# Kernel optimization log

Measured on AMD Instinct MI355X. Metric: run time of the kernel, lower is better.

## Reference

```python
import jax, jax.numpy as jnp
import numpy as np

B, T, H, O = 256, 512, 1024, 256


def setup_inputs() -> dict:
    key = jax.random.key(0)
    k0, k1, k2, k3, k4 = jax.random.split(key, 5)
    scale_ih = 1.0 / np.sqrt(1 + H)
    scale_ho = 1.0 / np.sqrt(H)
    return {
        "x": jax.random.normal(k0, (B, T), dtype=jnp.float32),
        "W_ih": jax.random.normal(k1, (1 + H, H), dtype=jnp.float32) * scale_ih,
        "b_ih": jax.random.normal(k2, (H,), dtype=jnp.float32) * scale_ih,
        "W_ho": jax.random.normal(k3, (H, O), dtype=jnp.float32) * scale_ho,
        "b_ho": jax.random.normal(k4, (O,), dtype=jnp.float32) * scale_ho,
    }


def reference(x, W_ih, b_ih, W_ho, b_ho):
    # Elman RNN cell: hidden = tanh(W_ih @ [x_t; h]); output = W_ho @ h_T.
    # Only the final timestep's output is returned by the original module,
    # so h2o is applied once to the final hidden state (identical math).
    batch = x.shape[0]
    h0 = jnp.zeros((batch, W_ih.shape[1]), dtype=x.dtype)

    def step(h, x_t):  # x_t: [B], h: [B, H]
        combined = jnp.concatenate([x_t[:, None], h], axis=1)  # [B, 1+H]
        h_new = jnp.tanh(combined @ W_ih + b_ih)               # [B, H]
        return h_new, None

    h_final, _ = jax.lax.scan(step, h0, x.T)  # scan over T
    return h_final @ W_ho + b_ho              # [B, O]
```

## Files before the change

kernel.cpp:

```cpp
#include <hip/hip_runtime.h>
#include <hip/hip_bf16.h>


#define Bsz 256
#define Tn  512
#define Hn  1024
#define On  256

typedef __attribute__((ext_vector_type(8))) _Float16 f16x8;
typedef __attribute__((ext_vector_type(4))) float f32x4;
typedef __attribute__((ext_vector_type(4))) int   i32x4;
typedef __attribute__((ext_vector_type(2))) int   i32x2;

__device__ __forceinline__ unsigned f2h(float f) {
    _Float16 h = (_Float16)f;
    union { _Float16 h; unsigned short s; } u; u.h = h;
    return (unsigned)u.s;
}

__device__ __forceinline__ f16x8 as_f16x8(i32x4 v) {
    union { i32x4 i; f16x8 h; } u; u.i = v; return u.h;
}

__device__ __forceinline__ float fast_tanh(float x) {
    float xc = fminf(fmaxf(x, -9.f), 9.f);
    float e  = __builtin_amdgcn_exp2f(xc * 2.8853900817779268f);
    return (e - 1.f) * __builtin_amdgcn_rcpf(e + 1.f);
}

#define MFMA_F16 __builtin_amdgcn_mfma_f32_16x16x32_f16

__device__ __forceinline__ void stage_quarter(const short* __restrict__ hsrc,
                                              short* __restrict__ htile,
                                              int row0, int cg, int kq,
                                              int lane, unsigned tag) {
    const int half = lane >> 5, gl = lane & 31, r0 = cg * 8;
    const short* a0 = hsrc + (size_t)(row0 + r0 + 0 + half) * Hn + kq * 256 + gl * 8;
    const short* a1 = hsrc + (size_t)(row0 + r0 + 2 + half) * Hn + kq * 256 + gl * 8;
    const short* a2 = hsrc + (size_t)(row0 + r0 + 4 + half) * Hn + kq * 256 + gl * 8;
    const short* a3 = hsrc + (size_t)(row0 + r0 + 6 + half) * Hn + kq * 256 + gl * 8;
    i32x4 t0, t1, t2, t3;
    for (;;) {
        asm volatile("global_load_dwordx4 %0, %1, off sc0 sc1"
                     : "=&v"(t0) : "v"(a0) : "memory");
        asm volatile("global_load_dwordx4 %0, %1, off sc0 sc1"
                     : "=&v"(t1) : "v"(a1) : "memory");
        asm volatile("global_load_dwordx4 %0, %1, off sc0 sc1"
                     : "=&v"(t2) : "v"(a2) : "memory");
        asm volatile("global_load_dwordx4 %0, %1, off sc0 sc1"
                     : "=&v"(t3) : "v"(a3) : "memory");
        asm volatile("s_waitcnt vmcnt(0)" ::: "memory");
        unsigned bad = 0;
#pragma unroll
        for (int e = 0; e < 4; ++e)
            bad |= (unsigned)(t0[e] ^ tag) | (unsigned)(t1[e] ^ tag) |
                   (unsigned)(t2[e] ^ tag) | (unsigned)(t3[e] ^ tag);
        if (!__any(bad & 1u)) break;
    }
    i32x4 tv[4] = {t0, t1, t2, t3};
#pragma unroll
    for (int p = 0; p < 4; ++p) {
        int row = r0 + 2 * p + half;
        int g   = kq * 32 + gl;
        int idx = row * 128 + (g ^ (row & 7));
        *(i32x4*)(htile + idx * 8) = tv[p];
    }
}

__global__ __launch_bounds__(512, 2) void rnn_kernel(
    const float* __restrict__ x,
    const float* __restrict__ W_ih,
    const float* __restrict__ b_ih,
    const float* __restrict__ W_ho,
    const float* __restrict__ b_ho,
    float* __restrict__ out,
    short* __restrict__ hbuf)
{
    const int tid  = threadIdx.x;
    const int lane = tid & 63;
    const int w    = tid >> 6;
    const int cg   = w >> 2;
    const int kq   = w & 3;
    const int q    = lane >> 4;
    const int n    = lane & 15;

    const int i = blockIdx.x & 15;
    const int j = blockIdx.x >> 4;
    const int colbase = j * 128 + cg * 64;
    const int owncol  = colbase + kq * 16 + 4 * q;
    const int row0    = i * 16;

    __shared__ float x_lds[16][Tn + 1];
    __shared__ short htile[16 * Hn];
    __shared__ float redbuf[2][8 * 3 * 256];
    __shared__ int   pairflag[4];

    if (tid < 4) pairflag[tid] = 0;

    for (int idx = tid; idx < 16 * Tn; idx += 512) {
        int r = idx >> 9, tt = idx & (Tn - 1);
        x_lds[r][tt] = x[(row0 + r) * Tn + tt];
    }

    f16x8 wfrag[32];
#pragma unroll
    for (int mt = 0; mt < 4; ++mt)
#pragma unroll
        for (int ks = 0; ks < 8; ++ks) {
#pragma unroll
            for (int e = 0; e < 8; ++e) {
                int k = kq * 256 + ks * 32 + q * 8 + e;
                wfrag[mt * 8 + ks][e] =
                    (_Float16)W_ih[(size_t)(1 + k) * Hn + colbase + mt * 16 + n];
            }
        }
    const float4 bias4 = *(const float4*)(b_ih + owncol);
    const float4 w04   = *(const float4*)(W_ih + owncol);

    __syncthreads();

    short* h0 = hbuf;
    short* h1 = hbuf + Bsz * Hn;
    const int swn   = n & 7;
    const int gbase = kq * 32;
    const int slot  = (q * 16 + n) * 4;
    const f32x4 zero4 = {0.f, 0.f, 0.f, 0.f};

    for (int t = 0; t < Tn; ++t) {
        const float xv = x_lds[n][t];
        f32x4 aown = {bias4.x + xv * w04.x, bias4.y + xv * w04.y,
                      bias4.z + xv * w04.z, bias4.w + xv * w04.w};
        f32x4 hv;

        if (t > 0) {
            stage_quarter((t & 1) ? h1 : h0, htile, row0, cg, kq, lane,
                          (unsigned)((t + 1) >> 1) & 1u);
            asm volatile("s_waitcnt lgkmcnt(0)" ::: "memory");
            if (lane == 0)
                __hip_atomic_fetch_add(&pairflag[kq], 1, __ATOMIC_RELAXED,
                                       __HIP_MEMORY_SCOPE_WORKGROUP);
            while (__hip_atomic_load(&pairflag[kq], __ATOMIC_RELAXED,
                                     __HIP_MEMORY_SCOPE_WORKGROUP) < 2 * t) {}
            asm volatile("" ::: "memory");

            f32x4 acc0 = (kq == 0) ? aown : zero4;
            f32x4 acc1 = (kq == 1) ? aown : zero4;
            f32x4 acc2 = (kq == 2) ? aown : zero4;
            f32x4 acc3 = (kq == 3) ? aown : zero4;
            const i32x4* lrow = (const i32x4*)(htile + n * Hn);
#pragma unroll
            for (int ks = 0; ks < 8; ++ks) {
                f16x8 b = as_f16x8(lrow[(gbase + ks * 4 + q) ^ swn]);
                acc0 = MFMA_F16(wfrag[0 * 8 + ks], b, acc0, 0, 0, 0);
                acc1 = MFMA_F16(wfrag[1 * 8 + ks], b, acc1, 0, 0, 0);
                acc2 = MFMA_F16(wfrag[2 * 8 + ks], b, acc2, 0, 0, 0);
                acc3 = MFMA_F16(wfrag[3 * 8 + ks], b, acc3, 0, 0, 0);
            }

            float* rb = redbuf[t & 1];
#define WRITE_PART(MT, ACC)                                                  \
            if (kq != MT) {                                                  \
                int src = (kq < MT) ? kq : kq - 1;                           \
                *(f32x4*)(rb + ((cg * 4 + MT) * 3 + src) * 256 + slot) = ACC;\
            }
            WRITE_PART(0, acc0)
            WRITE_PART(1, acc1)
            WRITE_PART(2, acc2)
            WRITE_PART(3, acc3)
#undef WRITE_PART
            __syncthreads();

            hv = (kq == 0) ? acc0 : (kq == 1) ? acc1 : (kq == 2) ? acc2 : acc3;
            const float* bp = rb + (cg * 4 + kq) * 3 * 256 + slot;
            f32x4 p0 = *(const f32x4*)(bp);
            f32x4 p1 = *(const f32x4*)(bp + 256);
            f32x4 p2 = *(const f32x4*)(bp + 512);
            hv = hv + p0 + p1 + p2;
        } else {
            hv = aown;
        }

        unsigned tagn = (unsigned)((t + 2) >> 1) & 1u;
        unsigned e0 = f2h(fast_tanh(hv[0])), e1 = f2h(fast_tanh(hv[1]));
        unsigned e2 = f2h(fast_tanh(hv[2])), e3 = f2h(fast_tanh(hv[3]));
        i32x2 pk;
        pk[0] = (int)(((e0 & ~1u) | tagn) | (e1 << 16));
        pk[1] = (int)(((e2 & ~1u) | tagn) | (e3 << 16));
        short* hdst = (((t + 1) & 1) ? h1 : h0) + (size_t)(row0 + n) * Hn + owncol;
        asm volatile("global_store_dwordx2 %0, %1, off sc0 sc1"
                     :: "v"(hdst), "v"(pk) : "memory");
    }

    stage_quarter(h0, htile, row0, cg, kq, lane, 0u);
    __syncthreads();

    f32x4 e0 = zero4, e1 = zero4;
    {
        const i32x4* lrow = (const i32x4*)(htile + n * Hn);
#pragma unroll
        for (int kk = 0; kk < 4; ++kk) {
            f16x8 af = as_f16x8(lrow[(w * 16 + kk * 4 + q) ^ swn]);
            f16x8 b0, b1;
#pragma unroll
            for (int e = 0; e < 8; ++e) {
                const float* wp = W_ho +
                    (size_t)(w * 128 + kk * 32 + q * 8 + e) * On + j * 32 + n;
                b0[e] = (_Float16)wp[0];
                b1[e] = (_Float16)wp[16];
            }
            e0 = MFMA_F16(af, b0, e0, 0, 0, 0);
            e1 = MFMA_F16(af, b1, e1, 0, 0, 0);
        }
    }
    {
        float* re = redbuf[0] + w * 528;
#pragma unroll
        for (int r = 0; r < 4; ++r) {
            re[(4 * q + r) * 33 + n]      = e0[r];
            re[(4 * q + r) * 33 + 16 + n] = e1[r];
        }
    }
    __syncthreads();
    {
        int r = tid >> 5, c = tid & 31;
        float s = b_ho[j * 32 + c];
#pragma unroll
        for (int w8 = 0; w8 < 8; ++w8)
            s += redbuf[0][w8 * 528 + r * 33 + c];
        out[(size_t)(row0 + r) * On + j * 32 + c] = s;
    }
}

extern "C" void kernel_launch(void* const* d_in, const int* in_sizes, int n_in,
                              void* d_out, int out_size, void* d_ws, size_t ws_size,
                              hipStream_t stream) {
    const float* x    = (const float*)d_in[0];
    const float* W_ih = (const float*)d_in[1];
    const float* b_ih = (const float*)d_in[2];
    const float* W_ho = (const float*)d_in[3];
    const float* b_ho = (const float*)d_in[4];
    float* out = (float*)d_out;

    size_t need = (size_t)2 * Bsz * Hn * sizeof(short);
    if (ws_size < need) return;

    short* hbuf = (short*)d_ws;

    rnn_kernel<<<128, 512, 0, stream>>>(x, W_ih, b_ih, W_ho, b_ho, out, hbuf);
}
```

Measured before the change: 1.080 ms.

## Gate hidden-state polling on per-wave progress flags before loading tiles

Adds a global per-(row group, column block, wave) progress counter that each wave stores after writing its hidden-state slice. Before staging a quarter of h, a wave polls 16 small flags with s_sleep backoff instead of repeatedly reloading the full 4x16B tagged tile. The goal is to cut memory traffic and contention from spinning on the large h buffer. The cost is an extra flag load round trip per step and a memset launch. Spin limits are added as a deadlock guard.

```diff
diff --git a/kernel.cpp b/kernel.cpp
--- a/kernel.cpp
+++ b/kernel.cpp
@@ -33,13 +33,27 @@
 __device__ __forceinline__ void stage_quarter(const short* __restrict__ hsrc,
                                               short* __restrict__ htile,
                                               int row0, int cg, int kq,
-                                              int lane, unsigned tag) {
+                                              int lane, unsigned tag,
+                                              const int* __restrict__ qflag,
+                                              int need) {
+    {
+        int fv, spin = 0;
+        for (;;) {
+            asm volatile("global_load_dword %0, %1, off sc0 sc1"
+                         : "=&v"(fv) : "v"(qflag) : "memory");
+            asm volatile("s_waitcnt vmcnt(0)" ::: "memory");
+            if (__all(fv >= need)) break;
+            __builtin_amdgcn_s_sleep(1);
+            if (++spin > (1 << 20)) break;
+        }
+    }
     const int half = lane >> 5, gl = lane & 31, r0 = cg * 8;
     const short* a0 = hsrc + (size_t)(row0 + r0 + 0 + half) * Hn + kq * 256 + gl * 8;
     const short* a1 = hsrc + (size_t)(row0 + r0 + 2 + half) * Hn + kq * 256 + gl * 8;
     const short* a2 = hsrc + (size_t)(row0 + r0 + 4 + half) * Hn + kq * 256 + gl * 8;
     const short* a3 = hsrc + (size_t)(row0 + r0 + 6 + half) * Hn + kq * 256 + gl * 8;
     i32x4 t0, t1, t2, t3;
+    int spin = 0;
     for (;;) {
         asm volatile("global_load_dwordx4 %0, %1, off sc0 sc1"
                      : "=&v"(t0) : "v"(a0) : "memory");
@@ -56,6 +70,7 @@
             bad |= (unsigned)(t0[e] ^ tag) | (unsigned)(t1[e] ^ tag) |
                    (unsigned)(t2[e] ^ tag) | (unsigned)(t3[e] ^ tag);
         if (!__any(bad & 1u)) break;
+        if (++spin > (1 << 20)) break;
     }
     i32x4 tv[4] = {t0, t1, t2, t3};
 #pragma unroll
@@ -74,7 +89,8 @@
     const float* __restrict__ W_ho,
     const float* __restrict__ b_ho,
     float* __restrict__ out,
-    short* __restrict__ hbuf)
+    short* __restrict__ hbuf,
+    int* __restrict__ flags)
 {
     const int tid  = threadIdx.x;
     const int lane = tid & 63;
@@ -90,6 +106,9 @@
     const int owncol  = colbase + kq * 16 + 4 * q;
     const int row0    = i * 16;
 
+    const int* qflag = flags + (i * 8 + 2 * kq) * 8 + (lane & 15);
+    int*       fdst  = flags + (i * 8 + j) * 8 + w;
+
     __shared__ float x_lds[16][Tn + 1];
     __shared__ short htile[16 * Hn];
     __shared__ float redbuf[2][8 * 3 * 256];
@@ -134,7 +153,7 @@
 
         if (t > 0) {
             stage_quarter((t & 1) ? h1 : h0, htile, row0, cg, kq, lane,
-                          (unsigned)((t + 1) >> 1) & 1u);
+                          (unsigned)((t + 1) >> 1) & 1u, qflag, t);
             asm volatile("s_waitcnt lgkmcnt(0)" ::: "memory");
             if (lane == 0)
                 __hip_atomic_fetch_add(&pairflag[kq], 1, __ATOMIC_RELAXED,
@@ -189,9 +208,14 @@
         short* hdst = (((t + 1) & 1) ? h1 : h0) + (size_t)(row0 + n) * Hn + owncol;
         asm volatile("global_store_dwordx2 %0, %1, off sc0 sc1"
                      :: "v"(hdst), "v"(pk) : "memory");
-    }
-
-    stage_quarter(h0, htile, row0, cg, kq, lane, 0u);
+        if (lane == 0) {
+            int fval = t + 1;
+            asm volatile("global_store_dword %0, %1, off sc0 sc1"
+                         :: "v"(fdst), "v"(fval) : "memory");
+        }
+    }
+
+    stage_quarter(h0, htile, row0, cg, kq, lane, 0u, qflag, Tn);
     __syncthreads();
 
     f32x4 e0 = zero4, e1 = zero4;
@@ -241,10 +265,15 @@
     const float* b_ho = (const float*)d_in[4];
     float* out = (float*)d_out;
 
-    size_t need = (size_t)2 * Bsz * Hn * sizeof(short);
-    if (ws_size < need) return;
-
-    short* hbuf = (short*)d_ws;
-
-    rnn_kernel<<<128, 512, 0, stream>>>(x, W_ih, b_ih, W_ho, b_ho, out, hbuf);
-}
+    size_t hbytes = (size_t)2 * Bsz * Hn * sizeof(short);
+    size_t fbytes = (size_t)16 * 8 * 8 * sizeof(int);
+    if (ws_size < hbytes + fbytes) return;
+
+    short* hbuf  = (short*)d_ws;
+    int*   flags = (int*)((char*)d_ws + hbytes);
+
+    hipMemsetAsync(flags, 0, fbytes, stream);
+
+    rnn_kernel<<<128, 512, 0, stream>>>(x, W_ih, b_ih, W_ho, b_ho, out,
+                                        hbuf, flags);
+}
```

Result: slower. 1.438 ms (+33.1%).
